# Kernel tuning notes

Hardware: AMD Instinct MI355X
Metric: run time of the kernel (lower is better)

## Reference

```python
import jax, jax.numpy as jnp
import numpy as np

B, S, HID = 4, 4096, 1024
HEADS, D = 8, 128          # head_dim = HID // HEADS
NSEG, SEGLEN = 16, 256     # SEGLEN = S // NSEG
E, I = 16, 512             # num_experts, intermediate_size


def setup_inputs() -> dict:
    key = jax.random.key(0)
    ks = jax.random.split(key, 8)
    return {
        "x": jax.random.normal(ks[0], (B, S, HID), jnp.float32),
        "W_mh": jax.random.normal(ks[1], (HID, HID), jnp.float32) * (1.0 / np.sqrt(HID)),
        "b_mh": jax.random.normal(ks[2], (HID,), jnp.float32) * 0.02,
        "W_merge": jax.random.normal(ks[3], (HID, HID), jnp.float32) * (1.0 / np.sqrt(HID)),
        "b_merge": jnp.zeros((HID,), jnp.float32),
        "expert_embeddings": jax.random.normal(ks[4], (D, E), jnp.float32) * (1.0 / np.sqrt(D)),
        "first_linear": jax.random.normal(ks[5], (E, I, D), jnp.float32) * (1.0 / np.sqrt(D)),
        "second_linear": jax.random.normal(ks[6], (E, D, I), jnp.float32) * (1.0 / np.sqrt(I)),
    }


def reference(x, W_mh, b_mh, W_merge, b_merge, expert_embeddings, first_linear, second_linear):
    # multi-head projection
    x = x @ W_mh.T + b_mh                                   # [B,S,HID]
    # split into segments/heads (faithful to torch reshape order)
    x = x.reshape(B, NSEG, SEGLEN, HEADS, D)                # [B,N,L,H,D]
    avg = jnp.mean(x, axis=2)                               # [B,N,H,D]
    # router: softmax over experts
    ew = jax.nn.softmax(jnp.einsum('bnhd,de->bnhe', avg, expert_embeddings), axis=-1)
    # merge expert weight matrices (equivalent to torch's broadcast-mul-sum)
    m1 = jnp.einsum('eid,bnhe->bnhid', first_linear, ew)    # [B,N,H,I,D]
    m2 = jnp.einsum('edi,bnhe->bnhdi', second_linear, ew)   # [B,N,H,D,I]
    # NOTE: torch uses reshape (not permute) here -> mixes seglen/head axes; replicate.
    xr = x.reshape(B, NSEG, HEADS, SEGLEN, D)               # [B,N,H,L,D]
    # causal shift: segment s uses weights from segment s-1
    x_causal = xr[:, 1:]
    h = jax.nn.relu(jnp.einsum('bnhld,bnhid->bnhli', x_causal, m1[:, :-1]))
    res = jnp.einsum('bnhli,bnhdi->bnhld', h, m2[:, :-1])   # [B,N-1,H,L,D]
    # segment 0 special case (no_grad in torch -> stop_gradient)
    h0 = jax.nn.relu(jnp.einsum('bhld,bhid->bhli', xr[:, 0], m1[:, 0]))
    r0 = jnp.einsum('bhli,bhdi->bhld', h0, m2[:, 0])
    r0 = jax.lax.stop_gradient(r0)[:, None]                 # [B,1,H,L,D]
    out = jnp.concatenate([r0, res], axis=1)                # [B,N,H,L,D]
    out = out.reshape(B, S, HEADS, D).reshape(B, S, HID)
    return out @ W_merge.T + b_merge
```

## Files before the change

### kernel.cpp

```cpp
#include <hip/hip_runtime.h>
#include <hip/hip_bf16.h>

typedef _Float16 f16;
typedef f16 f16x2 __attribute__((ext_vector_type(2)));
typedef f16 f16x4 __attribute__((ext_vector_type(4)));
typedef f16 f16x8 __attribute__((ext_vector_type(8)));
typedef float f32x2 __attribute__((ext_vector_type(2)));
typedef float f32x4 __attribute__((ext_vector_type(4)));

#define MFMA16(a, b, c) __builtin_amdgcn_mfma_f32_16x16x32_f16(a, b, c, 0, 0, 0)

__device__ __forceinline__ void glds16(const void* g, void* l) {
    __builtin_amdgcn_global_load_lds(
        (const __attribute__((address_space(1))) unsigned int*)g,
        (__attribute__((address_space(3))) unsigned int*)l, 16, 0, 0);
}

__global__ __launch_bounds__(256) void cvt_kernel(const float* __restrict__ s,
                                                  f16* __restrict__ d, int n) {
    int i = (blockIdx.x * 256 + threadIdx.x) * 8;
    if (i >= n) return;
    float4 a = *(const float4*)(s + i);
    float4 b = *(const float4*)(s + i + 4);
    f16x8 h;
    h[0] = (f16)a.x; h[1] = (f16)a.y; h[2] = (f16)a.z; h[3] = (f16)a.w;
    h[4] = (f16)b.x; h[5] = (f16)b.y; h[6] = (f16)b.z; h[7] = (f16)b.w;
    *(f16x8*)(d + i) = h;
}

template <bool OUT_F16>
__global__ __launch_bounds__(256) void gemm_bt_kernel(
    const f16* __restrict__ A16, const f16* __restrict__ Bw,
    const float* __restrict__ bias, void* __restrict__ C_, int M, int N, int K) {
    __shared__ f16 As[128 * 32];
    __shared__ f16 Bs[128 * 32];
    const int tid = threadIdx.x;
    const int lane = tid & 63;
    const int w = tid >> 6;
    const int nblk = N >> 7;
    const int cpx = (int)gridDim.x >> 3;
    const int logical = ((int)blockIdx.x & 7) * cpx + ((int)blockIdx.x >> 3);
    const int mb = logical / nblk, nb = logical % nblk;
    const int wm = w >> 1, wn = w & 1;
    const int q = lane >> 4, cl = lane & 15;

    const f16* Bbase = Bw + (size_t)nb * 128 * K;

    int srow[2], sg[2];
#pragma unroll
    for (int it = 0; it < 2; ++it) {
        int c = it * 256 + w * 64 + lane;
        srow[it] = c >> 2;
        sg[it] = (c & 3) ^ ((srow[it] >> 1) & 3);
    }
    const int qs = q ^ ((cl >> 1) & 3);

    f32x4 acc[4][4] = {};

#pragma unroll 1
    for (int kt = 0; kt < (K >> 5); ++kt) {
        const int k0 = kt << 5;
#pragma unroll
        for (int it = 0; it < 2; ++it) {
            glds16(Bbase + (size_t)srow[it] * K + k0 + sg[it] * 8,
                   &Bs[(it * 256 + w * 64) * 8]);
        }
#pragma unroll
        for (int it = 0; it < 2; ++it) {
            glds16(A16 + (size_t)(mb * 128 + srow[it]) * K + k0 + sg[it] * 8,
                   &As[(it * 256 + w * 64) * 8]);
        }
        __syncthreads();
        f16x8 af[4], bf[4];
#pragma unroll
        for (int mt = 0; mt < 4; ++mt)
            af[mt] = *(const f16x8*)&As[(wm * 64 + mt * 16 + cl) * 32 + qs * 8];
#pragma unroll
        for (int nt = 0; nt < 4; ++nt)
            bf[nt] = *(const f16x8*)&Bs[(wn * 64 + nt * 16 + cl) * 32 + qs * 8];
#pragma unroll
        for (int mt = 0; mt < 4; ++mt)
#pragma unroll
            for (int nt = 0; nt < 4; ++nt)
                acc[mt][nt] = MFMA16(af[mt], bf[nt], acc[mt][nt]);
        __syncthreads();
    }
    float bv[4];
#pragma unroll
    for (int nt = 0; nt < 4; ++nt) bv[nt] = bias[nb * 128 + wn * 64 + nt * 16 + cl];
#pragma unroll
    for (int mt = 0; mt < 4; ++mt) {
#pragma unroll
        for (int nt = 0; nt < 4; ++nt) {
            size_t gr = (size_t)(mb * 128 + wm * 64 + mt * 16 + q * 4);
            int gc = nb * 128 + wn * 64 + nt * 16 + cl;
#pragma unroll
            for (int r = 0; r < 4; ++r) {
                float v = acc[mt][nt][r] + bv[nt];
                if (OUT_F16)
                    ((f16*)C_)[(gr + r) * N + gc] = (f16)v;
                else
                    ((float*)C_)[(gr + r) * N + gc] = v;
            }
        }
    }
}

__global__ __launch_bounds__(256) void avg_kernel(const f16* __restrict__ X1h,
                                                  float* __restrict__ partial) {
    const int bn = blockIdx.x >> 2, rc = blockIdx.x & 3;
    const int tid = threadIdx.x;
    const f16* base = X1h + (size_t)bn * 262144 + (size_t)rc * 65536 + tid * 4;
    float s0 = 0.f, s1 = 0.f, s2 = 0.f, s3 = 0.f;
    for (int l = 0; l < 64; ++l) {
        f16x4 v = *(const f16x4*)(base + (size_t)l * 1024);
        s0 += (float)v[0]; s1 += (float)v[1]; s2 += (float)v[2]; s3 += (float)v[3];
    }
    const float sc = 1.f / 256.f;
    float4 o = make_float4(s0 * sc, s1 * sc, s2 * sc, s3 * sc);
    *(float4*)(partial + (size_t)(bn * 4 + rc) * 1024 + tid * 4) = o;
}

__global__ __launch_bounds__(64) void router_kernel(const float* __restrict__ partial,
                                                    const float* __restrict__ emb,
                                                    float* __restrict__ ew) {
    const int t = blockIdx.x;
    const int bn = t >> 3, h = t & 7;
    const int lane = threadIdx.x;
    float acc = 0.f;
    const float* p = partial + (size_t)bn * 4096 + h * 128;
    if (lane < 16) {
        for (int d = 0; d < 128; ++d) {
            float a = p[d] + p[d + 1024] + p[d + 2048] + p[d + 3072];
            acc = fmaf(a, emb[d * 16 + lane], acc);
        }
    }
    float m = acc;
#pragma unroll
    for (int o = 8; o; o >>= 1) m = fmaxf(m, __shfl_xor(m, o));
    float pr = __expf(acc - m);
    float s = pr;
#pragma unroll
    for (int o = 8; o; o >>= 1) s += __shfl_xor(s, o);
    if (lane < 16) ew[t * 16 + lane] = pr / s;
}

__global__ __launch_bounds__(256) void mix_kernel(const float* __restrict__ ew,
                                                  const float* __restrict__ FL,
                                                  const float* __restrict__ SL,
                                                  f16* __restrict__ m1h,
                                                  f16* __restrict__ m2h) {
    const int bid = blockIdx.x;
    const int which = bid >> 10;
    const int tg = (bid >> 6) & 15;
    const int chunk = bid & 63;
    const float* src = which ? SL : FL;
    f16* dst = which ? m2h : m1h;
    const int tid = threadIdx.x;
    const int e0 = chunk * 1024 + tid * 4;

    f32x4 fl[16];
#pragma unroll
    for (int e = 0; e < 16; ++e)
        fl[e] = *(const f32x4*)(src + (size_t)e * 65536 + e0);

    const float* wbase = ew + (size_t)tg * 32 * 16;
    float wc[16];
#pragma unroll
    for (int e = 0; e < 16; ++e) wc[e] = wbase[e];

#pragma unroll 1
    for (int tt = 0; tt < 32; ++tt) {
        float wn[16];
        if (tt < 31) {
#pragma unroll
            for (int e = 0; e < 16; ++e) wn[e] = wbase[(tt + 1) * 16 + e];
        }
        f32x4 a = {0.f, 0.f, 0.f, 0.f};
#pragma unroll
        for (int e = 0; e < 16; ++e) {
            a[0] = fmaf(wc[e], fl[e][0], a[0]);
            a[1] = fmaf(wc[e], fl[e][1], a[1]);
            a[2] = fmaf(wc[e], fl[e][2], a[2]);
            a[3] = fmaf(wc[e], fl[e][3], a[3]);
        }
        f16x4 h;
        h[0] = (f16)a[0]; h[1] = (f16)a[1]; h[2] = (f16)a[2]; h[3] = (f16)a[3];
        *(f16x4*)(dst + (size_t)(tg * 32 + tt) * 65536 + e0) = h;
        if (tt < 31) {
#pragma unroll
            for (int e = 0; e < 16; ++e) wc[e] = wn[e];
        }
    }
}

__device__ __forceinline__ void stage_w128(const f16* __restrict__ src, f16* lds,
                                           int w, int lane, int rowstride) {
#pragma unroll
    for (int it = 0; it < 8; ++it) {
        int cbase = it * 256 + w * 64;
        int c = cbase + lane;
        int row = c >> 4, pc = c & 15;
        int lc = pc ^ (row & 7);
        glds16(src + (size_t)row * rowstride + lc * 8, lds + cbase * 8);
    }
}

__global__ __launch_bounds__(256) void mlp_kernel(const f16* __restrict__ Xg,
                                                  const f16* __restrict__ m1h,
                                                  const f16* __restrict__ m2h,
                                                  f16* __restrict__ Yg) {
    __shared__ f16 Hs[128 * 128];
    __shared__ f16 Ws[128 * 128];
    const int cpx = (int)gridDim.x >> 3;
    const int logical = ((int)blockIdx.x & 7) * cpx + ((int)blockIdx.x >> 3);
    const int t = logical >> 1, lh = logical & 1;
    const int n = (t >> 3) & 15;
    const int tm = (n > 0) ? (t - 8) : t;
    const int tid = threadIdx.x;
    const int lane = tid & 63, w = tid >> 6;
    const int q = lane >> 4, cl = lane & 15;
    const int l0 = w * 32;

    const f16* Xsrc = Xg + (size_t)t * 32768 + lh * 16384;
    const f16* m1b = m1h + (size_t)tm * 65536;
    const f16* m2b = m2h + (size_t)tm * 65536;

    f16x8 xf[2][4];
#pragma unroll
    for (int lt = 0; lt < 2; ++lt) {
        int l = l0 + lt * 16 + cl;
#pragma unroll
        for (int ks = 0; ks < 4; ++ks)
            xf[lt][ks] = *(const f16x8*)(Xsrc + (size_t)l * 128 + ks * 32 + q * 8);
    }
    stage_w128(m1b, Ws, w, lane, 128);
    __syncthreads();

    f32x4 acc2[2][8] = {};
#pragma unroll 1
    for (int ic = 0; ic < 4; ++ic) {
#pragma unroll
        for (int it = 0; it < 8; ++it) {
            f16x8 af[4];
#pragma unroll
            for (int ks = 0; ks < 4; ++ks) {
                int r = it * 16 + cl;
                int ch = (ks * 4 + q) ^ (r & 7);
                af[ks] = *(const f16x8*)&Ws[r * 128 + ch * 8];
            }
            f32x4 a1[2] = {};
#pragma unroll
            for (int ks = 0; ks < 4; ++ks)
#pragma unroll
                for (int lt = 0; lt < 2; ++lt)
                    a1[lt] = MFMA16(af[ks], xf[lt][ks], a1[lt]);
            int ibase = it * 16 + q * 4;
            int ch = ibase >> 3;
            int sub = (q & 1) * 8;
#pragma unroll
            for (int lt = 0; lt < 2; ++lt) {
                int l = l0 + lt * 16 + cl;
                f16x4 hv;
                hv[0] = (f16)fmaxf(a1[lt][0], 0.f);
                hv[1] = (f16)fmaxf(a1[lt][1], 0.f);
                hv[2] = (f16)fmaxf(a1[lt][2], 0.f);
                hv[3] = (f16)fmaxf(a1[lt][3], 0.f);
                *(f16x4*)((char*)Hs + (size_t)l * 256 + ((ch ^ (l & 7)) << 4) + sub) = hv;
            }
        }
        __syncthreads();
        stage_w128(m2b + ic * 128, Ws, w, lane, 512);
        __syncthreads();

        f16x8 hf[2][4];
#pragma unroll
        for (int lt = 0; lt < 2; ++lt) {
            int l = l0 + lt * 16 + cl;
#pragma unroll
            for (int ks = 0; ks < 4; ++ks) {
                int ch = (ks * 4 + q) ^ (l & 7);
                hf[lt][ks] = *(const f16x8*)&Hs[l * 128 + ch * 8];
            }
        }
#pragma unroll
        for (int nt = 0; nt < 8; ++nt) {
            f16x8 bf[4];
#pragma unroll
            for (int ks = 0; ks < 4; ++ks) {
                int r = nt * 16 + cl;
                int ch = (ks * 4 + q) ^ (r & 7);
                bf[ks] = *(const f16x8*)&Ws[r * 128 + ch * 8];
            }
#pragma unroll
            for (int lt = 0; lt < 2; ++lt)
#pragma unroll
                for (int ks = 0; ks < 4; ++ks)
                    acc2[lt][nt] = MFMA16(hf[lt][ks], bf[ks], acc2[lt][nt]);
        }
        __syncthreads();
        if (ic < 3) {
            stage_w128(m1b + (size_t)(ic + 1) * 16384, Ws, w, lane, 128);
            __syncthreads();
        }
    }
    f16* Yb = Yg + (size_t)t * 32768 + lh * 16384;
#pragma unroll
    for (int lt = 0; lt < 2; ++lt) {
#pragma unroll
        for (int nt = 0; nt < 8; ++nt) {
            int lr = l0 + lt * 16 + q * 4;
            int d = nt * 16 + cl;
#pragma unroll
            for (int r = 0; r < 4; ++r)
                Yb[(size_t)(lr + r) * 128 + d] = (f16)acc2[lt][nt][r];
        }
    }
}

extern "C" void kernel_launch(void* const* d_in, const int* in_sizes, int n_in,
                              void* d_out, int out_size, void* d_ws, size_t ws_size,
                              hipStream_t stream) {
    const float* x    = (const float*)d_in[0];
    const float* W_mh = (const float*)d_in[1];
    const float* b_mh = (const float*)d_in[2];
    const float* W_mg = (const float*)d_in[3];
    const float* b_mg = (const float*)d_in[4];
    const float* emb  = (const float*)d_in[5];
    const float* FL   = (const float*)d_in[6];
    const float* SL   = (const float*)d_in[7];

    char* ws = (char*)d_ws;
    f16*   X1h  = (f16*)(ws + 0);
    f16*   m1h  = (f16*)(ws + 33554432);
    f16*   X0h  = (f16*)(ws + 33554432);
    f16*   m2h  = (f16*)(ws + 100663296);
    f16*   Wmhh = (f16*)(ws + 167772160);
    f16*   Wmgh = (f16*)(ws + 169869312);
    float* part = (float*)(ws + 171966464);
    float* ew   = (float*)(ws + 173015040);

    cvt_kernel<<<512, 256, 0, stream>>>(W_mh, Wmhh, 1048576);
    cvt_kernel<<<512, 256, 0, stream>>>(W_mg, Wmgh, 1048576);
    cvt_kernel<<<8192, 256, 0, stream>>>(x, X0h, 16777216);
    gemm_bt_kernel<true><<<1024, 256, 0, stream>>>(X0h, Wmhh, b_mh, X1h,
                                                   16384, 1024, 1024);
    avg_kernel<<<256, 256, 0, stream>>>(X1h, part);
    router_kernel<<<512, 64, 0, stream>>>(part, emb, ew);
    mix_kernel<<<2048, 256, 0, stream>>>(ew, FL, SL, m1h, m2h);
    mlp_kernel<<<1024, 256, 0, stream>>>(X1h, m1h, m2h, X1h);
    gemm_bt_kernel<false><<<1024, 256, 0, stream>>>(X1h, Wmgh, b_mg, d_out,
                                                    16384, 1024, 1024);
}
```

Before: 235.9 us.

## Double-buffer LDS tiles in GEMM to overlap global loads with MFMA

Converts the projection GEMM's shared-memory tiles to two ping-pong buffers. The next K-slice is prefetched via global_load_lds before computing the current one, and a partial vmcnt wait lets those loads overlap with the MFMA work instead of stalling every iteration. This doubles LDS use per block, which may lower occupancy, and relies on hand-placed waitcnt and barrier scheduling for correctness.

Measured after the change: 228.7 us. 1.03x faster.

```diff
diff --git a/kernel.cpp b/kernel.cpp
--- a/kernel.cpp
+++ b/kernel.cpp
@@ -32,8 +32,8 @@
 __global__ __launch_bounds__(256) void gemm_bt_kernel(
     const f16* __restrict__ A16, const f16* __restrict__ Bw,
     const float* __restrict__ bias, void* __restrict__ C_, int M, int N, int K) {
-    __shared__ f16 As[128 * 32];
-    __shared__ f16 Bs[128 * 32];
+    __shared__ f16 As[2][128 * 32];
+    __shared__ f16 Bs[2][128 * 32];
     const int tid = threadIdx.x;
     const int lane = tid & 63;
     const int w = tid >> 6;
@@ -54,36 +54,56 @@
         sg[it] = (c & 3) ^ ((srow[it] >> 1) & 3);
     }
     const int qs = q ^ ((cl >> 1) & 3);
+    const int KT = K >> 5;
 
     f32x4 acc[4][4] = {};
 
+#pragma unroll
+    for (int it = 0; it < 2; ++it)
+        glds16(Bbase + (size_t)srow[it] * K + sg[it] * 8,
+               &Bs[0][(it * 256 + w * 64) * 8]);
+#pragma unroll
+    for (int it = 0; it < 2; ++it)
+        glds16(A16 + (size_t)(mb * 128 + srow[it]) * K + sg[it] * 8,
+               &As[0][(it * 256 + w * 64) * 8]);
+
 #pragma unroll 1
-    for (int kt = 0; kt < (K >> 5); ++kt) {
-        const int k0 = kt << 5;
-#pragma unroll
-        for (int it = 0; it < 2; ++it) {
-            glds16(Bbase + (size_t)srow[it] * K + k0 + sg[it] * 8,
-                   &Bs[(it * 256 + w * 64) * 8]);
-        }
-#pragma unroll
-        for (int it = 0; it < 2; ++it) {
-            glds16(A16 + (size_t)(mb * 128 + srow[it]) * K + k0 + sg[it] * 8,
-                   &As[(it * 256 + w * 64) * 8]);
-        }
-        __syncthreads();
+    for (int kt = 0; kt < KT; ++kt) {
+        const int cur = kt & 1, nxt = cur ^ 1;
+        if (kt + 1 < KT) {
+            const int k1 = (kt + 1) << 5;
+#pragma unroll
+            for (int it = 0; it < 2; ++it)
+                glds16(Bbase + (size_t)srow[it] * K + k1 + sg[it] * 8,
+                       &Bs[nxt][(it * 256 + w * 64) * 8]);
+#pragma unroll
+            for (int it = 0; it < 2; ++it)
+                glds16(A16 + (size_t)(mb * 128 + srow[it]) * K + k1 + sg[it] * 8,
+                       &As[nxt][(it * 256 + w * 64) * 8]);
+            asm volatile("s_waitcnt vmcnt(4)" ::: "memory");
+        } else {
+            asm volatile("s_waitcnt vmcnt(0)" ::: "memory");
+        }
+        __builtin_amdgcn_sched_barrier(0);
+        __builtin_amdgcn_s_barrier();
+        __builtin_amdgcn_sched_barrier(0);
+
         f16x8 af[4], bf[4];
 #pragma unroll
         for (int mt = 0; mt < 4; ++mt)
-            af[mt] = *(const f16x8*)&As[(wm * 64 + mt * 16 + cl) * 32 + qs * 8];
+            af[mt] = *(const f16x8*)&As[cur][(wm * 64 + mt * 16 + cl) * 32 + qs * 8];
 #pragma unroll
         for (int nt = 0; nt < 4; ++nt)
-            bf[nt] = *(const f16x8*)&Bs[(wn * 64 + nt * 16 + cl) * 32 + qs * 8];
+            bf[nt] = *(const f16x8*)&Bs[cur][(wn * 64 + nt * 16 + cl) * 32 + qs * 8];
 #pragma unroll
         for (int mt = 0; mt < 4; ++mt)
 #pragma unroll
             for (int nt = 0; nt < 4; ++nt)
                 acc[mt][nt] = MFMA16(af[mt], bf[nt], acc[mt][nt]);
-        __syncthreads();
+
+        __builtin_amdgcn_sched_barrier(0);
+        __builtin_amdgcn_s_barrier();
+        __builtin_amdgcn_sched_barrier(0);
     }
     float bv[4];
 #pragma unroll
```
